# Kernel tuning notes

Measured on AMD Instinct MI355X. Metric: run time of the kernel, lower is better.

## Reference

```python
import jax, jax.numpy as jnp
import numpy as np

B, H1, H2, D, C = 4096, 32, 32, 32, 64


def setup_inputs() -> dict:
    key = jax.random.key(0)
    k1, k2, k3 = jax.random.split(key, 3)
    x = jax.random.normal(k1, (B, H1, D), dtype=jnp.float32)
    y = jax.random.normal(k2, (B, H2, D), dtype=jnp.float32)
    # glorot-uniform-ish kernel of shape (compress_dim, H1, H2)
    limit = float(np.sqrt(6.0 / (H1 + H2)))
    kernel = jax.random.uniform(k3, (C, H1, H2), dtype=jnp.float32,
                                minval=-limit, maxval=limit)
    return {"x": x, "y": y, "kernel": kernel}


def reference(x, y, kernel):
    # Original math: outer[b,i,j,d] = x[b,i,d]*y[b,j,d];
    # output_mat[b,c,d] = sum_{i,j} outer[b,i,j,d] * kernel[c,i,j]
    # Expressed as a fused bilinear contraction (avoids the [B,H1,H2,D] tensor):
    # first fold kernel into y per compress channel, then contract with x.
    t = jnp.einsum('cij,bjd->bcid', kernel, y)       # [B,C,H1,D]
    output_mat = jnp.einsum('bid,bcid->bcd', x, t)   # [B,C,D]
    final_output = jnp.sum(output_mat, axis=-1)      # [B,C]
    return (output_mat, final_output)
```

## Files before the change

### kernel.cpp

```cpp
#include <hip/hip_runtime.h>
#include <hip/hip_bf16.h>


typedef __attribute__((ext_vector_type(8))) short short8;
typedef __attribute__((ext_vector_type(4))) float f32x4;

__device__ __forceinline__ unsigned short f2bf_rne(float f) {
    union { float f; unsigned u; } w; w.f = f;
    return (unsigned short)((w.u + 0x7FFFu + ((w.u >> 16) & 1u)) >> 16);
}

__global__ __launch_bounds__(256) void kswz_kernel(const float* __restrict__ kern,
                                                   short* __restrict__ kswz) {
    int idx  = blockIdx.x * 256 + threadIdx.x;
    int lane = idx & 63;
    int nt   = (idx >> 6) & 3;
    int s    = idx >> 8;
    int c    = nt * 16 + (lane & 15);
    int jb   = (lane >> 4) * 8;
    const float* src = kern + c * 1024 + s * 32 + jb;
    short8 v;
#pragma unroll
    for (int t = 0; t < 8; ++t) v[t] = (short)f2bf_rne(src[t]);
    *(short8*)(kswz + (size_t)idx * 8) = v;
}

__global__ __launch_bounds__(256) void cin_main(const float* __restrict__ x,
                                                const float* __restrict__ y,
                                                const short* __restrict__ kswz,
                                                float* __restrict__ out_mat,
                                                float* __restrict__ out_fin) {
    __shared__ float xs[8 * 1024];

    const int tid  = threadIdx.x;
    const int wave = tid >> 6;
    const int lane = tid & 63;
    const int quad = lane >> 4;
    const int n16  = lane & 15;
    const int b_blk = blockIdx.x * 8;

    {
        const float4* xg = (const float4*)(x + (size_t)b_blk * 1024);
        float4* xs4 = (float4*)xs;
#pragma unroll
        for (int i = 0; i < 8; ++i) xs4[tid + 256 * i] = xg[tid + 256 * i];
    }
    __syncthreads();

    const int b0 = b_blk + wave * 2;

    float yv[4][8];
#pragma unroll
    for (int mt = 0; mt < 4; ++mt) {
        const int b = b0 + (mt >> 1);
        const int d = n16 + 16 * (mt & 1);
        const float* yp = y + (size_t)b * 1024 + (quad * 8) * 32 + d;
#pragma unroll
        for (int t = 0; t < 8; ++t) yv[mt][t] = yp[t * 32];
    }

    f32x4 acc[4][4];
#pragma unroll
    for (int mt = 0; mt < 4; ++mt)
#pragma unroll
        for (int nt = 0; nt < 4; ++nt) acc[mt][nt] = (f32x4){0.f, 0.f, 0.f, 0.f};

    const short8* kp = (const short8*)kswz;

    for (int s = 0; s < 32; ++s) {
        short8 bfrag[4];
#pragma unroll
        for (int nt = 0; nt < 4; ++nt) bfrag[nt] = kp[(s * 4 + nt) * 64 + lane];

#pragma unroll
        for (int mt = 0; mt < 4; ++mt) {
            const int bl = wave * 2 + (mt >> 1);
            const int d  = n16 + 16 * (mt & 1);
            const float xv = xs[bl * 1024 + s * 32 + d];

            union { short8 s8; __hip_bfloat162 h2[4]; } af;
#pragma unroll
            for (int p = 0; p < 4; ++p) {
                float2 pr = make_float2(xv * yv[mt][2 * p], xv * yv[mt][2 * p + 1]);
                af.h2[p] = __float22bfloat162_rn(pr);
            }
#pragma unroll
            for (int nt = 0; nt < 4; ++nt)
                acc[mt][nt] = __builtin_amdgcn_mfma_f32_16x16x32_bf16(
                    af.s8, bfrag[nt], acc[mt][nt], 0, 0, 0);
        }
    }

#pragma unroll
    for (int mt = 0; mt < 4; ++mt) {
        const int b = b0 + (mt >> 1);
        const int dbase = 16 * (mt & 1) + quad * 4;
#pragma unroll
        for (int nt = 0; nt < 4; ++nt) {
            const int c = nt * 16 + n16;
            *(f32x4*)(out_mat + (size_t)b * 2048 + c * 32 + dbase) = acc[mt][nt];
        }
    }

#pragma unroll
    for (int a = 0; a < 2; ++a) {
        const int b = b0 + a;
#pragma unroll
        for (int nt = 0; nt < 4; ++nt) {
            float f = 0.f;
#pragma unroll
            for (int t = 0; t < 4; ++t) f += acc[2 * a][nt][t] + acc[2 * a + 1][nt][t];
            f += __shfl_xor(f, 16);
            f += __shfl_xor(f, 32);
            if (lane < 16) out_fin[(size_t)b * 64 + nt * 16 + n16] = f;
        }
    }
}

extern "C" void kernel_launch(void* const* d_in, const int* in_sizes, int n_in,
                              void* d_out, int out_size, void* d_ws, size_t ws_size,
                              hipStream_t stream) {
    const float* x    = (const float*)d_in[0];
    const float* y    = (const float*)d_in[1];
    const float* kern = (const float*)d_in[2];
    float* out_mat = (float*)d_out;
    float* out_fin = (float*)d_out + 4096 * 64 * 32;
    short* kswz = (short*)d_ws;

    kswz_kernel<<<32, 256, 0, stream>>>(kern, kswz);
    cin_main<<<512, 256, 0, stream>>>(x, y, kswz, out_mat, out_fin);
}
```

Before: 112.5 us.

## Split compress channels across waves, halve batch per block, prefetch kernel fragments

Each block now covers 4 batches instead of 8. Pairs of waves split the 64 compress channels, so each wave holds half the accumulators, and the grid doubles to 1024 blocks. The swizzled kernel layout is interleaved so each wave loads its two B fragments from adjacent 16-byte chunks. The main loop is fully unrolled and software-pipelined, prefetching the next step's kernel fragments and x values from LDS, with the syncthreads moved later. The aim is more parallelism and occupancy and hidden load latency, at the cost of redundant y loads and more per-thread register pressure from the unrolling.

```diff
diff --git a/kernel.cpp b/kernel.cpp
--- a/kernel.cpp
+++ b/kernel.cpp
@@ -12,42 +12,44 @@
 
 __global__ __launch_bounds__(256) void kswz_kernel(const float* __restrict__ kern,
                                                    short* __restrict__ kswz) {
-    int idx  = blockIdx.x * 256 + threadIdx.x;
-    int lane = idx & 63;
-    int nt   = (idx >> 6) & 3;
-    int s    = idx >> 8;
-    int c    = nt * 16 + (lane & 15);
+    int f    = blockIdx.x * 256 + threadIdx.x;
+    int ntl  = f & 1;
+    int lane = (f >> 1) & 63;
+    int nth  = (f >> 7) & 1;
+    int s    = f >> 8;
+    int c    = (nth * 2 + ntl) * 16 + (lane & 15);
     int jb   = (lane >> 4) * 8;
     const float* src = kern + c * 1024 + s * 32 + jb;
     short8 v;
 #pragma unroll
     for (int t = 0; t < 8; ++t) v[t] = (short)f2bf_rne(src[t]);
-    *(short8*)(kswz + (size_t)idx * 8) = v;
+    *(short8*)(kswz + (size_t)f * 8) = v;
 }
 
-__global__ __launch_bounds__(256) void cin_main(const float* __restrict__ x,
-                                                const float* __restrict__ y,
-                                                const short* __restrict__ kswz,
-                                                float* __restrict__ out_mat,
-                                                float* __restrict__ out_fin) {
-    __shared__ float xs[8 * 1024];
+__global__ __launch_bounds__(256, 4) void cin_main(const float* __restrict__ x,
+                                                   const float* __restrict__ y,
+                                                   const short* __restrict__ kswz,
+                                                   float* __restrict__ out_mat,
+                                                   float* __restrict__ out_fin) {
+    __shared__ float xs[4 * 1024];
 
     const int tid  = threadIdx.x;
     const int wave = tid >> 6;
     const int lane = tid & 63;
     const int quad = lane >> 4;
     const int n16  = lane & 15;
-    const int b_blk = blockIdx.x * 8;
+    const int b_blk = blockIdx.x * 4;
+    const int bpair = wave >> 1;
+    const int nth   = wave & 1;
 
     {
         const float4* xg = (const float4*)(x + (size_t)b_blk * 1024);
         float4* xs4 = (float4*)xs;
 #pragma unroll
-        for (int i = 0; i < 8; ++i) xs4[tid + 256 * i] = xg[tid + 256 * i];
+        for (int i = 0; i < 4; ++i) xs4[tid + 256 * i] = xg[tid + 256 * i];
     }
-    __syncthreads();
 
-    const int b0 = b_blk + wave * 2;
+    const int b0 = b_blk + bpair * 2;
 
     float yv[4][8];
 #pragma unroll
@@ -59,36 +61,53 @@
         for (int t = 0; t < 8; ++t) yv[mt][t] = yp[t * 32];
     }
 
-    f32x4 acc[4][4];
+    f32x4 acc[4][2];
 #pragma unroll
     for (int mt = 0; mt < 4; ++mt)
 #pragma unroll
-        for (int nt = 0; nt < 4; ++nt) acc[mt][nt] = (f32x4){0.f, 0.f, 0.f, 0.f};
+        for (int ntl = 0; ntl < 2; ++ntl) acc[mt][ntl] = (f32x4){0.f, 0.f, 0.f, 0.f};
 
-    const short8* kp = (const short8*)kswz;
+    const char* kb = (const char*)kswz + (size_t)(nth * 2048 + lane * 32);
+    int xoff[4];
+#pragma unroll
+    for (int mt = 0; mt < 4; ++mt)
+        xoff[mt] = (bpair * 2 + (mt >> 1)) * 1024 + n16 + 16 * (mt & 1);
 
+    __syncthreads();
+
+    short8 bc0 = *(const short8*)(kb);
+    short8 bc1 = *(const short8*)(kb + 16);
+    float xc[4];
+#pragma unroll
+    for (int mt = 0; mt < 4; ++mt) xc[mt] = xs[xoff[mt]];
+
+#pragma unroll
     for (int s = 0; s < 32; ++s) {
-        short8 bfrag[4];
+        short8 bn0, bn1;
+        float xn[4];
+        if (s < 31) {
+            bn0 = *(const short8*)(kb + (s + 1) * 4096);
+            bn1 = *(const short8*)(kb + (s + 1) * 4096 + 16);
 #pragma unroll
-        for (int nt = 0; nt < 4; ++nt) bfrag[nt] = kp[(s * 4 + nt) * 64 + lane];
+            for (int mt = 0; mt < 4; ++mt) xn[mt] = xs[xoff[mt] + (s + 1) * 32];
+        }
 
 #pragma unroll
         for (int mt = 0; mt < 4; ++mt) {
-            const int bl = wave * 2 + (mt >> 1);
-            const int d  = n16 + 16 * (mt & 1);
-            const float xv = xs[bl * 1024 + s * 32 + d];
-
             union { short8 s8; __hip_bfloat162 h2[4]; } af;
+            const float xv = xc[mt];
 #pragma unroll
             for (int p = 0; p < 4; ++p) {
                 float2 pr = make_float2(xv * yv[mt][2 * p], xv * yv[mt][2 * p + 1]);
                 af.h2[p] = __float22bfloat162_rn(pr);
             }
+            acc[mt][0] = __builtin_amdgcn_mfma_f32_16x16x32_bf16(af.s8, bc0, acc[mt][0], 0, 0, 0);
+            acc[mt][1] = __builtin_amdgcn_mfma_f32_16x16x32_bf16(af.s8, bc1, acc[mt][1], 0, 0, 0);
+        }
+
+        bc0 = bn0; bc1 = bn1;
 #pragma unroll
-            for (int nt = 0; nt < 4; ++nt)
-                acc[mt][nt] = __builtin_amdgcn_mfma_f32_16x16x32_bf16(
-                    af.s8, bfrag[nt], acc[mt][nt], 0, 0, 0);
-        }
+        for (int mt = 0; mt < 4; ++mt) xc[mt] = xn[mt];
     }
 
 #pragma unroll
@@ -96,9 +115,9 @@
         const int b = b0 + (mt >> 1);
         const int dbase = 16 * (mt & 1) + quad * 4;
 #pragma unroll
-        for (int nt = 0; nt < 4; ++nt) {
-            const int c = nt * 16 + n16;
-            *(f32x4*)(out_mat + (size_t)b * 2048 + c * 32 + dbase) = acc[mt][nt];
+        for (int ntl = 0; ntl < 2; ++ntl) {
+            const int c = (nth * 2 + ntl) * 16 + n16;
+            *(f32x4*)(out_mat + (size_t)b * 2048 + c * 32 + dbase) = acc[mt][ntl];
         }
     }
 
@@ -106,13 +125,13 @@
     for (int a = 0; a < 2; ++a) {
         const int b = b0 + a;
 #pragma unroll
-        for (int nt = 0; nt < 4; ++nt) {
+        for (int ntl = 0; ntl < 2; ++ntl) {
             float f = 0.f;
 #pragma unroll
-            for (int t = 0; t < 4; ++t) f += acc[2 * a][nt][t] + acc[2 * a + 1][nt][t];
+            for (int t = 0; t < 4; ++t) f += acc[2 * a][ntl][t] + acc[2 * a + 1][ntl][t];
             f += __shfl_xor(f, 16);
             f += __shfl_xor(f, 32);
-            if (lane < 16) out_fin[(size_t)b * 64 + nt * 16 + n16] = f;
+            if (lane < 16) out_fin[(size_t)b * 64 + (nth * 2 + ntl) * 16 + n16] = f;
         }
     }
 }
@@ -128,5 +147,5 @@
     short* kswz = (short*)d_ws;
 
     kswz_kernel<<<32, 256, 0, stream>>>(kern, kswz);
-    cin_main<<<512, 256, 0, stream>>>(x, y, kswz, out_mat, out_fin);
+    cin_main<<<1024, 256, 0, stream>>>(x, y, kswz, out_mat, out_fin);
 }
```

Result: faster. 109.4 us (-2.7%).

## Switch to fp16 MFMA with packed products and LDS-staged kernel tiles

Applied to the files above, without the earlier changes.

Moves the operands from bf16 to fp16. The x*y products are now formed with packed half-precision multiplies instead of an fp32 multiply followed by a bf16 conversion. Kernel weight fragments are staged into double-buffered LDS through global_load_lds, with a rotating start offset per block to spread traffic, instead of being read straight from global memory on every step. This aims to cut conversion ALU work and global load latency in the inner loop, at the cost of extra LDS, a per-chunk barrier and different rounding (fp16 products with round-toward-zero conversion).

```diff
diff --git a/kernel.cpp b/kernel.cpp
--- a/kernel.cpp
+++ b/kernel.cpp
@@ -1,17 +1,23 @@
 #include <hip/hip_runtime.h>
-#include <hip/hip_bf16.h>
+#include <hip/hip_fp16.h>
 
 
+typedef __attribute__((ext_vector_type(8))) _Float16 half8;
+typedef __attribute__((ext_vector_type(2))) __fp16 fp16x2;
+typedef __attribute__((ext_vector_type(4))) float f32x4;
 typedef __attribute__((ext_vector_type(8))) short short8;
-typedef __attribute__((ext_vector_type(4))) float f32x4;
 
-__device__ __forceinline__ unsigned short f2bf_rne(float f) {
-    union { float f; unsigned u; } w; w.f = f;
-    return (unsigned short)((w.u + 0x7FFFu + ((w.u >> 16) & 1u)) >> 16);
+__device__ __forceinline__ unsigned int dup_h(float f) {
+    union { fp16x2 h; unsigned int u; } w;
+    w.h = __builtin_amdgcn_cvt_pkrtz(f, f);
+    return w.u;
+}
+__device__ __forceinline__ fp16x2 pk2(float a, float b) {
+    return __builtin_amdgcn_cvt_pkrtz(a, b);
 }
 
 __global__ __launch_bounds__(256) void kswz_kernel(const float* __restrict__ kern,
-                                                   short* __restrict__ kswz) {
+                                                   unsigned short* __restrict__ kswz) {
     int idx  = blockIdx.x * 256 + threadIdx.x;
     int lane = idx & 63;
     int nt   = (idx >> 6) & 3;
@@ -19,18 +25,25 @@
     int c    = nt * 16 + (lane & 15);
     int jb   = (lane >> 4) * 8;
     const float* src = kern + c * 1024 + s * 32 + jb;
-    short8 v;
+    union { half8 h; short8 s8; } v;
 #pragma unroll
-    for (int t = 0; t < 8; ++t) v[t] = (short)f2bf_rne(src[t]);
-    *(short8*)(kswz + (size_t)idx * 8) = v;
+    for (int t = 0; t < 8; ++t) v.h[t] = (_Float16)src[t];
+    *(short8*)(kswz + (size_t)idx * 8) = v.s8;
 }
 
-__global__ __launch_bounds__(256) void cin_main(const float* __restrict__ x,
-                                                const float* __restrict__ y,
-                                                const short* __restrict__ kswz,
-                                                float* __restrict__ out_mat,
-                                                float* __restrict__ out_fin) {
-    __shared__ float xs[8 * 1024];
+__device__ __forceinline__ void gld_lds16(const void* g, void* l) {
+    __builtin_amdgcn_global_load_lds(
+        (const __attribute__((address_space(1))) unsigned int*)g,
+        (__attribute__((address_space(3))) unsigned int*)l, 16, 0, 0);
+}
+
+__global__ __launch_bounds__(256, 2) void cin_main(const float* __restrict__ x,
+                                                   const float* __restrict__ y,
+                                                   const unsigned short* __restrict__ kswz,
+                                                   float* __restrict__ out_mat,
+                                                   float* __restrict__ out_fin) {
+    __shared__ unsigned int xs[8 * 1024];
+    __shared__ __align__(16) unsigned short kb[2][8192];
 
     const int tid  = threadIdx.x;
     const int wave = tid >> 6;
@@ -38,25 +51,36 @@
     const int quad = lane >> 4;
     const int n16  = lane & 15;
     const int b_blk = blockIdx.x * 8;
+    const int cq0   = blockIdx.x & 7;
+
+#pragma unroll
+    for (int r = 0; r < 4; ++r)
+        gld_lds16(kswz + (size_t)cq0 * 8192 + (r * 256 + tid) * 8,
+                  &kb[0][r * 2048 + wave * 512]);
 
     {
-        const float4* xg = (const float4*)(x + (size_t)b_blk * 1024);
-        float4* xs4 = (float4*)xs;
+        const float4* xg4 = (const float4*)(x + (size_t)b_blk * 1024);
 #pragma unroll
-        for (int i = 0; i < 8; ++i) xs4[tid + 256 * i] = xg[tid + 256 * i];
+        for (int r = 0; r < 8; ++r) {
+            int i4 = r * 256 + tid;
+            float4 v = xg4[i4];
+            uint4 w;
+            w.x = dup_h(v.x); w.y = dup_h(v.y); w.z = dup_h(v.z); w.w = dup_h(v.w);
+            *(uint4*)&xs[i4 * 4] = w;
+        }
     }
-    __syncthreads();
 
-    const int b0 = b_blk + wave * 2;
-
-    float yv[4][8];
+    const int bpair = wave;
+    const int b0 = b_blk + bpair * 2;
+    fp16x2 yv2[4][4];
 #pragma unroll
     for (int mt = 0; mt < 4; ++mt) {
         const int b = b0 + (mt >> 1);
         const int d = n16 + 16 * (mt & 1);
         const float* yp = y + (size_t)b * 1024 + (quad * 8) * 32 + d;
 #pragma unroll
-        for (int t = 0; t < 8; ++t) yv[mt][t] = yp[t * 32];
+        for (int p = 0; p < 4; ++p)
+            yv2[mt][p] = pk2(yp[(2 * p) * 32], yp[(2 * p + 1) * 32]);
     }
 
     f32x4 acc[4][4];
@@ -65,30 +89,45 @@
 #pragma unroll
         for (int nt = 0; nt < 4; ++nt) acc[mt][nt] = (f32x4){0.f, 0.f, 0.f, 0.f};
 
-    const short8* kp = (const short8*)kswz;
+    int xoff[4];
+#pragma unroll
+    for (int mt = 0; mt < 4; ++mt)
+        xoff[mt] = (bpair * 2 + (mt >> 1)) * 1024 + n16 + 16 * (mt & 1);
 
-    for (int s = 0; s < 32; ++s) {
-        short8 bfrag[4];
+    __syncthreads();
+
+    for (int p8 = 0; p8 < 8; ++p8) {
+        if (p8 < 7) {
+            const int cn = (cq0 + p8 + 1) & 7;
+            unsigned short* dst = &kb[(p8 + 1) & 1][0];
 #pragma unroll
-        for (int nt = 0; nt < 4; ++nt) bfrag[nt] = kp[(s * 4 + nt) * 64 + lane];
+            for (int r = 0; r < 4; ++r)
+                gld_lds16(kswz + (size_t)cn * 8192 + (r * 256 + tid) * 8,
+                          dst + r * 2048 + wave * 512);
+        }
 
+        const unsigned short* kbase = &kb[p8 & 1][0];
+        const int sb = ((cq0 + p8) & 7) * 4;
 #pragma unroll
-        for (int mt = 0; mt < 4; ++mt) {
-            const int bl = wave * 2 + (mt >> 1);
-            const int d  = n16 + 16 * (mt & 1);
-            const float xv = xs[bl * 1024 + s * 32 + d];
-
-            union { short8 s8; __hip_bfloat162 h2[4]; } af;
-#pragma unroll
-            for (int p = 0; p < 4; ++p) {
-                float2 pr = make_float2(xv * yv[mt][2 * p], xv * yv[mt][2 * p + 1]);
-                af.h2[p] = __float22bfloat162_rn(pr);
-            }
+        for (int k = 0; k < 4; ++k) {
+            half8 bf[4];
 #pragma unroll
             for (int nt = 0; nt < 4; ++nt)
-                acc[mt][nt] = __builtin_amdgcn_mfma_f32_16x16x32_bf16(
-                    af.s8, bfrag[nt], acc[mt][nt], 0, 0, 0);
+                bf[nt] = *(const half8*)(kbase + ((k * 4 + nt) * 64 + lane) * 8);
+#pragma unroll
+            for (int mt = 0; mt < 4; ++mt) {
+                union { unsigned int u; fp16x2 h; } xv;
+                xv.u = xs[xoff[mt] + (sb + k) * 32];
+                union { half8 h8; fp16x2 h2[4]; } af;
+#pragma unroll
+                for (int p = 0; p < 4; ++p) af.h2[p] = xv.h * yv2[mt][p];
+#pragma unroll
+                for (int nt = 0; nt < 4; ++nt)
+                    acc[mt][nt] = __builtin_amdgcn_mfma_f32_16x16x32_f16(
+                        af.h8, bf[nt], acc[mt][nt], 0, 0, 0);
+            }
         }
+        __syncthreads();
     }
 
 #pragma unroll
@@ -125,7 +164,7 @@
     const float* kern = (const float*)d_in[2];
     float* out_mat = (float*)d_out;
     float* out_fin = (float*)d_out + 4096 * 64 * 32;
-    short* kswz = (short*)d_ws;
+    unsigned short* kswz = (unsigned short*)d_ws;
 
     kswz_kernel<<<32, 256, 0, stream>>>(kern, kswz);
     cin_main<<<512, 256, 0, stream>>>(x, y, kswz, out_mat, out_fin);
```

After: 100.8 us. -10.4%, faster.
